# Kernel tuning notes

Hardware: AMD Instinct MI355X
Metric: run time of the kernel (lower is better)

Reference implementation:

```python
import jax, jax.numpy as jnp
import numpy as np

EMBED_DIM = 768
NUM_HEADS = 12
HEAD_DIM = EMBED_DIM // NUM_HEADS


def setup_inputs() -> dict:
    key = jax.random.key(0)
    k_x, k_wqkv, k_bqkv, k_wp, k_bp = jax.random.split(key, 5)
    B, N, C = 4, 2048, EMBED_DIM
    # torch nn.Linear init scale ~ 1/sqrt(fan_in); use small normal for numerics
    s = 1.0 / np.sqrt(C)
    return {
        "x": jax.random.normal(k_x, (B, N, C), dtype=jnp.float32),
        "w_qkv": jax.random.normal(k_wqkv, (3 * C, C), dtype=jnp.float32) * s,  # torch [out,in]
        "b_qkv": jax.random.normal(k_bqkv, (3 * C,), dtype=jnp.float32) * s,
        "w_proj": jax.random.normal(k_wp, (C, C), dtype=jnp.float32) * s,
        "b_proj": jax.random.normal(k_bp, (C,), dtype=jnp.float32) * s,
    }


def reference(x, w_qkv, b_qkv, w_proj, b_proj):
    B, N, C = x.shape
    H, D = NUM_HEADS, HEAD_DIM
    scale = 1.0 / np.sqrt(D)
    # qkv linear: x @ W.T + b  -> [B,N,3C]
    qkv = jnp.einsum("bnc,oc->bno", x, w_qkv) + b_qkv
    qkv = qkv.reshape(B, N, 3, H, D).transpose(2, 0, 3, 1, 4)  # [3,B,H,N,D]
    q, k, v = qkv[0], qkv[1], qkv[2]
    attn = jnp.einsum("bhnd,bhmd->bhnm", q, k) * scale  # [B,H,N,N]
    attn = jax.nn.softmax(attn, axis=-1)
    out = jnp.einsum("bhnm,bhmd->bhnd", attn, v)  # [B,H,N,D]
    out = out.transpose(0, 2, 1, 3).reshape(B, N, C)
    return jnp.einsum("bnc,oc->bno", out, w_proj) + b_proj
```

## Files before the change

kernel.cpp:

```cpp
#include <hip/hip_runtime.h>
#include <hip/hip_bf16.h>
#include <math.h>

#define EMBED 768
#define NHEAD 12
#define HDIM 64
#define SEQ 2048
#define BATCH 4

typedef __hip_bfloat16 bf16;
typedef __attribute__((ext_vector_type(8))) short bf16x8;
typedef __attribute__((ext_vector_type(4))) short s16x4;
typedef __attribute__((ext_vector_type(4))) float f32x4;
typedef __attribute__((ext_vector_type(2))) unsigned int u32x2;

__device__ inline float b2f(bf16 v) { return __bfloat162float(v); }
__device__ inline bf16 f2b(float v) { return __float2bfloat16(v); }
__device__ inline unsigned pk2(float a, float b) {
  return (unsigned)__bfloat16_as_ushort(f2b(a)) |
         ((unsigned)__bfloat16_as_ushort(f2b(b)) << 16);
}

__device__ inline void gl_lds16(const bf16* g, bf16* l) {
  __builtin_amdgcn_global_load_lds(
      (const __attribute__((address_space(1))) void*)g,
      (__attribute__((address_space(3))) void*)l, 16, 0, 0);
}

#define NX4  (BATCH * SEQ * EMBED / 4)
#define NWQ4 (3 * EMBED * EMBED / 4)
#define NWP4 (EMBED * EMBED / 4)

__global__ __launch_bounds__(256) void cvt_all(
    const float* __restrict__ x, const float* __restrict__ wq,
    const float* __restrict__ wp, bf16* __restrict__ xb,
    bf16* __restrict__ wqb, bf16* __restrict__ wpb) {
  int i = blockIdx.x * 256 + threadIdx.x;
  const float* src;
  bf16* dst;
  int k;
  if (i < NX4) {
    src = x; dst = xb; k = i;
  } else if (i < NX4 + NWQ4) {
    src = wq; dst = wqb; k = i - NX4;
  } else if (i < NX4 + NWQ4 + NWP4) {
    src = wp; dst = wpb; k = i - NX4 - NWQ4;
  } else {
    return;
  }
  float4 v = ((const float4*)src)[k];
  s16x4 o;
  o[0] = (short)__bfloat16_as_ushort(f2b(v.x));
  o[1] = (short)__bfloat16_as_ushort(f2b(v.y));
  o[2] = (short)__bfloat16_as_ushort(f2b(v.z));
  o[3] = (short)__bfloat16_as_ushort(f2b(v.w));
  *(s16x4*)(dst + 4 * (size_t)k) = o;
}

template <int MODE>
__global__ __launch_bounds__(256) void gemm_mfma(
    const bf16* __restrict__ A, const bf16* __restrict__ W,
    const float* __restrict__ bias, float* __restrict__ outF,
    bf16* __restrict__ outQ, bf16* __restrict__ outK, bf16* __restrict__ outV,
    int M, int N, int K) {
  __shared__ bf16 As[128][32];
  __shared__ bf16 Bs[128][32];
  const int t = threadIdx.x;
  const int w = t >> 6;
  const int lane = t & 63;
  const int g = lane >> 4, c = lane & 15;
  const int m0 = blockIdx.y * 128, n0 = blockIdx.x * 128;
  const int wr = (w >> 1) * 64;
  const int wc = (w & 1) * 64;

  const int srow = lane >> 2;
  const int sseg = (lane & 3) * 8;

  f32x4 acc[4][4] = {};

  for (int k0 = 0; k0 < K; k0 += 32) {
#pragma unroll
    for (int i = 0; i < 2; i++) {
      int r = w * 32 + i * 16;
      gl_lds16(A + (size_t)(m0 + r + srow) * K + k0 + sseg, &As[r][0]);
      gl_lds16(W + (size_t)(n0 + r + srow) * K + k0 + sseg, &Bs[r][0]);
    }
    __syncthreads();

    bf16x8 xf[4], wf[4];
#pragma unroll
    for (int j = 0; j < 4; j++)
      xf[j] = *(const bf16x8*)&As[wr + j * 16 + c][g * 8];
#pragma unroll
    for (int i = 0; i < 4; i++)
      wf[i] = *(const bf16x8*)&Bs[wc + i * 16 + c][g * 8];
#pragma unroll
    for (int i = 0; i < 4; i++)
#pragma unroll
      for (int j = 0; j < 4; j++)
        acc[i][j] = __builtin_amdgcn_mfma_f32_16x16x32_bf16(wf[i], xf[j],
                                                            acc[i][j], 0, 0, 0);
    __syncthreads();
  }

#pragma unroll
  for (int i = 0; i < 4; i++) {
    const int ob = n0 + wc + i * 16 + g * 4;
    const f32x4 bv = *(const f32x4*)&bias[ob];
    int which = 0, hh = 0, d0 = 0;
    if (MODE == 0) {
      which = ob / EMBED;
      int rem = ob - which * EMBED;
      hh = rem >> 6;
      d0 = rem & 63;
    }
#pragma unroll
    for (int j = 0; j < 4; j++) {
      const int m = m0 + wr + j * 16 + c;
      f32x4 v = acc[i][j] + bv;
      if (MODE == 0) {
        const int bb = m >> 11, n = m & 2047;
        const size_t bh = (size_t)bb * NHEAD + hh;
        if (which == 0) {
          s16x4 q4;
#pragma unroll
          for (int r = 0; r < 4; r++)
            q4[r] = (short)__bfloat16_as_ushort(f2b(v[r] * 0.1803368801f));
          *(s16x4*)&outQ[(bh * SEQ + n) * HDIM + d0] = q4;
        } else if (which == 1) {
          s16x4 k4;
#pragma unroll
          for (int r = 0; r < 4; r++)
            k4[r] = (short)__bfloat16_as_ushort(f2b(v[r]));
          *(s16x4*)&outK[(bh * SEQ + n) * HDIM + d0] = k4;
        } else {
#pragma unroll
          for (int r = 0; r < 4; r++)
            outV[(bh * HDIM + d0 + r) * SEQ + n] = f2b(v[r]);
        }
      } else {
        *(f32x4*)&outF[(size_t)m * N + ob] = v;
      }
    }
  }
}

__global__ __launch_bounds__(256, 4) void attn_mfma(
    const bf16* __restrict__ Q, const bf16* __restrict__ Kk,
    const bf16* __restrict__ V, bf16* __restrict__ O) {
  __shared__ bf16 Ks[64 * 64];
  __shared__ bf16 Vts[64 * 64];
  __shared__ bf16 Pt[8][16 * 72];

  const int blk = blockIdx.x;
  const int bh = blk >> 4;
  const int qt = blk & 15;
  const int bb = bh / NHEAD;
  const int h = bh % NHEAD;
  const int t = threadIdx.x;
  const int lane = t & 63;
  const int w = t >> 6;
  const int g = lane >> 4;
  const int c = lane & 15;
  const size_t base = (size_t)bh * SEQ * HDIM;
  const int mb0 = qt * 128 + w * 16;
  const int mb1 = mb0 + 64;

  const int r8 = lane >> 3;
  const int l8 = lane & 7;
  const int gch = l8 ^ (r8 & 7);
  const int q0 = w * 2, q1 = w * 2 + 1;

  bf16x8 qa[2][2];
#pragma unroll
  for (int kh = 0; kh < 2; kh++) {
    qa[0][kh] = *(const bf16x8*)(Q + base + (size_t)(mb0 + c) * HDIM + kh * 32 + g * 8);
    qa[1][kh] = *(const bf16x8*)(Q + base + (size_t)(mb1 + c) * HDIM + kh * 32 + g * 8);
  }

  bf16x8 ones;
#pragma unroll
  for (int i = 0; i < 8; i++) ones[i] = (short)0x3F80;

  f32x4 o[2][4] = {};
  f32x4 o_l[2] = {};

  gl_lds16(Kk + base + (size_t)(q0 * 8 + r8) * HDIM + gch * 8, &Ks[q0 * 8 * 64]);
  gl_lds16(Kk + base + (size_t)(q1 * 8 + r8) * HDIM + gch * 8, &Ks[q1 * 8 * 64]);
  gl_lds16(V + base + (size_t)(q0 * 8 + r8) * SEQ + gch * 8, &Vts[q0 * 8 * 64]);
  gl_lds16(V + base + (size_t)(q1 * 8 + r8) * SEQ + gch * 8, &Vts[q1 * 8 * 64]);
  __syncthreads();

  bf16* const Pt0 = Pt[w * 2];
  bf16* const Pt1 = Pt[w * 2 + 1];

  for (int jt = 0; jt < SEQ / 64; jt++) {
    f32x4 s[2][4] = {};
#pragma unroll
    for (int nt = 0; nt < 4; nt++) {
#pragma unroll
      for (int kh = 0; kh < 2; kh++) {
        bf16x8 kb = *(const bf16x8*)&Ks[(nt * 16 + c) * 64 + ((kh * 4 + g) ^ (c & 7)) * 8];
        s[0][nt] = __builtin_amdgcn_mfma_f32_16x16x32_bf16(kb, qa[0][kh], s[0][nt], 0, 0, 0);
        s[1][nt] = __builtin_amdgcn_mfma_f32_16x16x32_bf16(kb, qa[1][kh], s[1][nt], 0, 0, 0);
      }
    }

    __syncthreads();
    if (jt + 1 < SEQ / 64) {
      const int jb = (jt + 1) * 64;
      gl_lds16(Kk + base + (size_t)(jb + q0 * 8 + r8) * HDIM + gch * 8, &Ks[q0 * 8 * 64]);
      gl_lds16(Kk + base + (size_t)(jb + q1 * 8 + r8) * HDIM + gch * 8, &Ks[q1 * 8 * 64]);
    }

#pragma unroll
    for (int nt = 0; nt < 4; nt++) {
      float a0 = __builtin_amdgcn_exp2f(s[0][nt][0]);
      float a1 = __builtin_amdgcn_exp2f(s[0][nt][1]);
      float a2 = __builtin_amdgcn_exp2f(s[0][nt][2]);
      float a3 = __builtin_amdgcn_exp2f(s[0][nt][3]);
      u32x2 pw0 = {pk2(a0, a1), pk2(a2, a3)};
      *(u32x2*)&Pt0[c * 72 + nt * 16 + g * 4] = pw0;
      float b0 = __builtin_amdgcn_exp2f(s[1][nt][0]);
      float b1 = __builtin_amdgcn_exp2f(s[1][nt][1]);
      float b2 = __builtin_amdgcn_exp2f(s[1][nt][2]);
      float b3 = __builtin_amdgcn_exp2f(s[1][nt][3]);
      u32x2 pw1 = {pk2(b0, b1), pk2(b2, b3)};
      *(u32x2*)&Pt1[c * 72 + nt * 16 + g * 4] = pw1;
    }
    bf16x8 pb[2][2];
    pb[0][0] = *(const bf16x8*)&Pt0[c * 72 + g * 8];
    pb[0][1] = *(const bf16x8*)&Pt0[c * 72 + 32 + g * 8];
    pb[1][0] = *(const bf16x8*)&Pt1[c * 72 + g * 8];
    pb[1][1] = *(const bf16x8*)&Pt1[c * 72 + 32 + g * 8];

#pragma unroll
    for (int dt = 0; dt < 4; dt++) {
      bf16x8 vb0 = *(const bf16x8*)&Vts[(dt * 16 + c) * 64 + ((0 + g) ^ (c & 7)) * 8];
      bf16x8 vb1 = *(const bf16x8*)&Vts[(dt * 16 + c) * 64 + ((4 + g) ^ (c & 7)) * 8];
      o[0][dt] = __builtin_amdgcn_mfma_f32_16x16x32_bf16(vb0, pb[0][0], o[0][dt], 0, 0, 0);
      o[0][dt] = __builtin_amdgcn_mfma_f32_16x16x32_bf16(vb1, pb[0][1], o[0][dt], 0, 0, 0);
      o[1][dt] = __builtin_amdgcn_mfma_f32_16x16x32_bf16(vb0, pb[1][0], o[1][dt], 0, 0, 0);
      o[1][dt] = __builtin_amdgcn_mfma_f32_16x16x32_bf16(vb1, pb[1][1], o[1][dt], 0, 0, 0);
    }
    o_l[0] = __builtin_amdgcn_mfma_f32_16x16x32_bf16(ones, pb[0][0], o_l[0], 0, 0, 0);
    o_l[0] = __builtin_amdgcn_mfma_f32_16x16x32_bf16(ones, pb[0][1], o_l[0], 0, 0, 0);
    o_l[1] = __builtin_amdgcn_mfma_f32_16x16x32_bf16(ones, pb[1][0], o_l[1], 0, 0, 0);
    o_l[1] = __builtin_amdgcn_mfma_f32_16x16x32_bf16(ones, pb[1][1], o_l[1], 0, 0, 0);

    __syncthreads();
    if (jt + 1 < SEQ / 64) {
      const int jb = (jt + 1) * 64;
      gl_lds16(V + base + (size_t)(q0 * 8 + r8) * SEQ + jb + gch * 8, &Vts[q0 * 8 * 64]);
      gl_lds16(V + base + (size_t)(q1 * 8 + r8) * SEQ + jb + gch * 8, &Vts[q1 * 8 * 64]);
    }
  }

#pragma unroll
  for (int grp = 0; grp < 2; grp++) {
    const float inv = __builtin_amdgcn_rcpf(o_l[grp][0]);
    const int mb = grp ? mb1 : mb0;
    const size_t rowoff = ((size_t)bb * SEQ + mb + c) * EMBED + h * 64 + g * 4;
#pragma unroll
    for (int dt = 0; dt < 4; dt++) {
      s16x4 ov;
#pragma unroll
      for (int r = 0; r < 4; r++)
        ov[r] = (short)__bfloat16_as_ushort(f2b(o[grp][dt][r] * inv));
      *(s16x4*)&O[rowoff + dt * 16] = ov;
    }
  }
}

extern "C" void kernel_launch(void* const* d_in, const int* in_sizes, int n_in,
                              void* d_out, int out_size, void* d_ws,
                              size_t ws_size, hipStream_t stream) {
  const float* x      = (const float*)d_in[0];
  const float* w_qkv  = (const float*)d_in[1];
  const float* b_qkv  = (const float*)d_in[2];
  const float* w_proj = (const float*)d_in[3];
  const float* b_proj = (const float*)d_in[4];

  const size_t per = (size_t)BATCH * NHEAD * SEQ * HDIM;
  bf16* Qp = (bf16*)d_ws;
  bf16* Kp = Qp + per;
  bf16* Vp = Kp + per;
  bf16* xb = Vp + per;
  bf16* wqkvb = xb + per;
  bf16* wprojb = wqkvb + (size_t)3 * EMBED * EMBED;
  bf16* AO = xb;

  const int ncvt = NX4 + NWQ4 + NWP4;
  cvt_all<<<dim3((ncvt + 255) / 256), 256, 0, stream>>>(x, w_qkv, w_proj, xb,
                                                        wqkvb, wprojb);

  dim3 g1(2304 / 128, 8192 / 128);
  gemm_mfma<0><<<g1, 256, 0, stream>>>(xb, wqkvb, b_qkv, nullptr, Qp, Kp, Vp,
                                       BATCH * SEQ, 3 * EMBED, EMBED);

  attn_mfma<<<dim3(BATCH * NHEAD * (SEQ / 128)), 256, 0, stream>>>(Qp, Kp, Vp, AO);

  dim3 g2(768 / 128, 8192 / 128);
  gemm_mfma<1><<<g2, 256, 0, stream>>>(AO, wprojb, b_proj, (float*)d_out,
                                       nullptr, nullptr, nullptr, BATCH * SEQ,
                                       EMBED, EMBED);
}
```

Measured before the change: 237.4 us.

## Double-buffer K/V tiles in LDS and raise wave priority around MFMA loops

Splits the K and V shared-memory tiles into two ping-pong buffers. The next tile's global-to-LDS loads are issued at the top of each iteration, so they overlap the current tile's QK and PV MFMA work. The two barriers per iteration become one. s_setprio is also raised around the MFMA blocks to favour matrix-issuing waves. The trade-off is more LDS per block (about 50KB), which can lower resident blocks per CU below the launch-bounds target of four.

```diff
diff --git a/kernel.cpp b/kernel.cpp
--- a/kernel.cpp
+++ b/kernel.cpp
@@ -148,8 +148,8 @@
 __global__ __launch_bounds__(256, 4) void attn_mfma(
     const bf16* __restrict__ Q, const bf16* __restrict__ Kk,
     const bf16* __restrict__ V, bf16* __restrict__ O) {
-  __shared__ bf16 Ks[64 * 64];
-  __shared__ bf16 Vts[64 * 64];
+  __shared__ bf16 Ks[2][64 * 64];
+  __shared__ bf16 Vts[2][64 * 64];
   __shared__ bf16 Pt[8][16 * 72];
 
   const int blk = blockIdx.x;
@@ -185,33 +185,42 @@
   f32x4 o[2][4] = {};
   f32x4 o_l[2] = {};
 
-  gl_lds16(Kk + base + (size_t)(q0 * 8 + r8) * HDIM + gch * 8, &Ks[q0 * 8 * 64]);
-  gl_lds16(Kk + base + (size_t)(q1 * 8 + r8) * HDIM + gch * 8, &Ks[q1 * 8 * 64]);
-  gl_lds16(V + base + (size_t)(q0 * 8 + r8) * SEQ + gch * 8, &Vts[q0 * 8 * 64]);
-  gl_lds16(V + base + (size_t)(q1 * 8 + r8) * SEQ + gch * 8, &Vts[q1 * 8 * 64]);
+  gl_lds16(Kk + base + (size_t)(q0 * 8 + r8) * HDIM + gch * 8, &Ks[0][q0 * 8 * 64]);
+  gl_lds16(Kk + base + (size_t)(q1 * 8 + r8) * HDIM + gch * 8, &Ks[0][q1 * 8 * 64]);
+  gl_lds16(V + base + (size_t)(q0 * 8 + r8) * SEQ + gch * 8, &Vts[0][q0 * 8 * 64]);
+  gl_lds16(V + base + (size_t)(q1 * 8 + r8) * SEQ + gch * 8, &Vts[0][q1 * 8 * 64]);
   __syncthreads();
 
   bf16* const Pt0 = Pt[w * 2];
   bf16* const Pt1 = Pt[w * 2 + 1];
 
   for (int jt = 0; jt < SEQ / 64; jt++) {
+    const int p = jt & 1;
+
+    if (jt + 1 < SEQ / 64) {
+      const int jb = (jt + 1) * 64;
+      gl_lds16(Kk + base + (size_t)(jb + q0 * 8 + r8) * HDIM + gch * 8,
+               &Ks[p ^ 1][q0 * 8 * 64]);
+      gl_lds16(Kk + base + (size_t)(jb + q1 * 8 + r8) * HDIM + gch * 8,
+               &Ks[p ^ 1][q1 * 8 * 64]);
+      gl_lds16(V + base + (size_t)(q0 * 8 + r8) * SEQ + jb + gch * 8,
+               &Vts[p ^ 1][q0 * 8 * 64]);
+      gl_lds16(V + base + (size_t)(q1 * 8 + r8) * SEQ + jb + gch * 8,
+               &Vts[p ^ 1][q1 * 8 * 64]);
+    }
+
     f32x4 s[2][4] = {};
+    __builtin_amdgcn_s_setprio(1);
 #pragma unroll
     for (int nt = 0; nt < 4; nt++) {
 #pragma unroll
       for (int kh = 0; kh < 2; kh++) {
-        bf16x8 kb = *(const bf16x8*)&Ks[(nt * 16 + c) * 64 + ((kh * 4 + g) ^ (c & 7)) * 8];
+        bf16x8 kb = *(const bf16x8*)&Ks[p][(nt * 16 + c) * 64 + ((kh * 4 + g) ^ (c & 7)) * 8];
         s[0][nt] = __builtin_amdgcn_mfma_f32_16x16x32_bf16(kb, qa[0][kh], s[0][nt], 0, 0, 0);
         s[1][nt] = __builtin_amdgcn_mfma_f32_16x16x32_bf16(kb, qa[1][kh], s[1][nt], 0, 0, 0);
       }
     }
-
-    __syncthreads();
-    if (jt + 1 < SEQ / 64) {
-      const int jb = (jt + 1) * 64;
-      gl_lds16(Kk + base + (size_t)(jb + q0 * 8 + r8) * HDIM + gch * 8, &Ks[q0 * 8 * 64]);
-      gl_lds16(Kk + base + (size_t)(jb + q1 * 8 + r8) * HDIM + gch * 8, &Ks[q1 * 8 * 64]);
-    }
+    __builtin_amdgcn_s_setprio(0);
 
 #pragma unroll
     for (int nt = 0; nt < 4; nt++) {
@@ -234,10 +243,11 @@
     pb[1][0] = *(const bf16x8*)&Pt1[c * 72 + g * 8];
     pb[1][1] = *(const bf16x8*)&Pt1[c * 72 + 32 + g * 8];
 
+    __builtin_amdgcn_s_setprio(1);
 #pragma unroll
     for (int dt = 0; dt < 4; dt++) {
-      bf16x8 vb0 = *(const bf16x8*)&Vts[(dt * 16 + c) * 64 + ((0 + g) ^ (c & 7)) * 8];
-      bf16x8 vb1 = *(const bf16x8*)&Vts[(dt * 16 + c) * 64 + ((4 + g) ^ (c & 7)) * 8];
+      bf16x8 vb0 = *(const bf16x8*)&Vts[p][(dt * 16 + c) * 64 + ((0 + g) ^ (c & 7)) * 8];
+      bf16x8 vb1 = *(const bf16x8*)&Vts[p][(dt * 16 + c) * 64 + ((4 + g) ^ (c & 7)) * 8];
       o[0][dt] = __builtin_amdgcn_mfma_f32_16x16x32_bf16(vb0, pb[0][0], o[0][dt], 0, 0, 0);
       o[0][dt] = __builtin_amdgcn_mfma_f32_16x16x32_bf16(vb1, pb[0][1], o[0][dt], 0, 0, 0);
       o[1][dt] = __builtin_amdgcn_mfma_f32_16x16x32_bf16(vb0, pb[1][0], o[1][dt], 0, 0, 0);
@@ -247,13 +257,9 @@
     o_l[0] = __builtin_amdgcn_mfma_f32_16x16x32_bf16(ones, pb[0][1], o_l[0], 0, 0, 0);
     o_l[1] = __builtin_amdgcn_mfma_f32_16x16x32_bf16(ones, pb[1][0], o_l[1], 0, 0, 0);
     o_l[1] = __builtin_amdgcn_mfma_f32_16x16x32_bf16(ones, pb[1][1], o_l[1], 0, 0, 0);
-
-    __syncthreads();
-    if (jt + 1 < SEQ / 64) {
-      const int jb = (jt + 1) * 64;
-      gl_lds16(V + base + (size_t)(q0 * 8 + r8) * SEQ + jb + gch * 8, &Vts[q0 * 8 * 64]);
-      gl_lds16(V + base + (size_t)(q1 * 8 + r8) * SEQ + jb + gch * 8, &Vts[q1 * 8 * 64]);
-    }
+    __builtin_amdgcn_s_setprio(0);
+
+    if (jt + 1 < SEQ / 64) __syncthreads();
   }
 
 #pragma unroll
```

Result: no change. 239.1 us (+0.7%).
